# Kernel optimization log

Hardware: AMD Instinct MI355X
Metric: run time of the kernel (lower is better)

Reference implementation:

```python
import jax, jax.numpy as jnp
import numpy as np

N_NODES = 100000
N_EDGES = 1600000
D = 128


def gcn_conv(x, src, dst, ew, W, b, num_nodes):
    """PyG GCNConv: self-loops (weight 1), symmetric deg^{-1/2} normalization,
    linear transform (no bias) then scatter-add aggregation at dst, bias after."""
    loop = jnp.arange(num_nodes)
    s = jnp.concatenate([src, loop])
    d = jnp.concatenate([dst, loop])
    w = jnp.concatenate([ew, jnp.ones((num_nodes,), dtype=x.dtype)])
    deg = jax.ops.segment_sum(w, d, num_segments=num_nodes)
    dinv = jnp.where(deg > 0, jax.lax.rsqrt(deg), 0.0).astype(x.dtype)
    norm = dinv[s] * w * dinv[d]                      # [E+N]
    h = x @ W                                          # [N, out]
    msgs = h[s] * norm[:, None]                        # [E+N, out]
    return jax.ops.segment_sum(msgs, d, num_segments=num_nodes) + b


def setup_inputs() -> dict:
    key = jax.random.key(0)
    ks = jax.random.split(key, 7)
    x = jax.random.normal(ks[0], (N_NODES, D), dtype=jnp.float32)
    edge_index = jax.random.randint(ks[1], (2, N_EDGES), 0, N_NODES, dtype=jnp.int64)
    edge_weight = jax.random.uniform(ks[2], (N_EDGES,), dtype=jnp.float32)
    scale = 1.0 / np.sqrt(D)
    W1 = jax.random.normal(ks[3], (D, D), dtype=jnp.float32) * scale
    b1 = jax.random.normal(ks[4], (D,), dtype=jnp.float32) * 0.01
    W2 = jax.random.normal(ks[5], (D, D), dtype=jnp.float32) * scale
    b2 = jax.random.normal(ks[6], (D,), dtype=jnp.float32) * 0.01
    return {"x": x, "edge_index": edge_index, "edge_weight": edge_weight,
            "W1": W1, "b1": b1, "W2": W2, "b2": b2}


def reference(x, edge_index, edge_weight, W1, b1, W2, b2):
    src, dst = edge_index[0], edge_index[1]
    n = x.shape[0]
    h = gcn_conv(x, src, dst, edge_weight, W1, b1, n)
    h = jax.nn.relu(h)
    h = gcn_conv(h, src, dst, edge_weight, W2, b2, n)
    return jax.nn.relu(h)
```

## Files before the change

kernel.cpp:

```cpp
#include <hip/hip_runtime.h>

#define D 128
#define CAP 64
#define NBSHIFT 7
#define BNODES 128
#define NGRP 8
#define SUBCAP 384

typedef __attribute__((ext_vector_type(8))) short bf16x8;
typedef __attribute__((ext_vector_type(4))) float f32x4;

__device__ __forceinline__ ushort f2bf(float f) {
    uint u = __float_as_uint(f);
    return (ushort)((u + 0x7FFFu + ((u >> 16) & 1u)) >> 16);
}

__global__ __launch_bounds__(256) void k_prep(const float* __restrict__ W1,
                                              const float* __restrict__ W2,
                                              ushort* __restrict__ Wt1,
                                              ushort* __restrict__ Wt2,
                                              int* scnt, int nsc) {
    int i = blockIdx.x * 256 + threadIdx.x;
    if (i < nsc) scnt[i] = 0;
    if (i < 2 * D * D) {
        const float* W = (i < D * D) ? W1 : W2;
        ushort* Wt     = (i < D * D) ? Wt1 : Wt2;
        int j = i & (D * D - 1);
        int k = j >> 7, nn = j & 127;
        Wt[nn * D + k] = f2bf(W[k * D + nn]);
    }
}

__global__ __launch_bounds__(256) void k_bin(const int* __restrict__ src,
                                             const int* __restrict__ dst,
                                             const float* __restrict__ ew,
                                             int* scnt,
                                             uint2* __restrict__ rec, int nE) {
    int e = blockIdx.x * 256 + threadIdx.x;
    if (e >= nE) return;
    int d = dst[e];
    int b = d >> NBSHIFT;
    int g = blockIdx.x & (NGRP - 1);
    int cell = b * NGRP + g;
    int pos = atomicAdd(&scnt[cell], 1);
    if (pos < SUBCAP) {
        uint q = (uint)__float2int_rn(ew[e] * 32767.0f);
        rec[(size_t)cell * SUBCAP + pos] =
            make_uint2(((uint)src[e] << 15) | q, (uint)(d & (BNODES - 1)));
    }
}

__global__ __launch_bounds__(256) void k_build(const uint2* __restrict__ rec,
                                               const int* __restrict__ scnt,
                                               uint* __restrict__ bucket,
                                               int* __restrict__ cnt,
                                               float* __restrict__ dinv, int n) {
    __shared__ uint rows[BNODES * (CAP + 1)];
    __shared__ int  lcnt[BNODES];
    const int tid = threadIdx.x;
    const int b   = blockIdx.x;

    if (tid < BNODES) lcnt[tid] = 0;
    __syncthreads();

#pragma unroll
    for (int g = 0; g < NGRP; ++g) {
        int cell = b * NGRP + g;
        int c = min(scnt[cell], SUBCAP);
        for (int i = tid; i < c; i += 256) {
            uint2 r = rec[(size_t)cell * SUBCAP + i];
            int nl = (int)r.y;
            int p = atomicAdd(&lcnt[nl], 1);
            if (p < CAP) rows[nl * (CAP + 1) + p] = r.x;
        }
    }
    __syncthreads();

    if (tid < BNODES) {
        int node = b * BNODES + tid;
        if (node < n) {
            int c = min(lcnt[tid], CAP);
            float wsum = 0.f;
            for (int i = 0; i < c; ++i)
                wsum += (float)(rows[tid * (CAP + 1) + i] & 32767u);
            dinv[node] = rsqrtf(1.0f + wsum * (1.0f / 32767.0f));
            cnt[node]  = c;
        }
    }
    __syncthreads();

    for (int i = tid; i < BNODES * CAP; i += 256) {
        int nl = i >> 6, sl = i & (CAP - 1);
        int node = b * BNODES + nl;
        if (node < n) bucket[(size_t)node * CAP + sl] = rows[nl * (CAP + 1) + sl];
    }
}

template <bool IN_BF16>
__global__ __launch_bounds__(256) void k_gemm(const void* __restrict__ Xv,
                                              const ushort* __restrict__ Wt,
                                              ushort* __restrict__ H, int n) {
    __shared__ ushort Xs[64][136];
    __shared__ ushort Ws[128][136];
    const int tid  = threadIdx.x;
    const int row0 = blockIdx.x * 64;

#pragma unroll
    for (int p = 0; p < 8; ++p) {
        int f = (p * 256 + tid) * 8;
        int nn = f >> 7, kk = f & 127;
        *(uint4*)(&Ws[nn][kk]) = *(const uint4*)(Wt + f);
    }
    if (IN_BF16) {
        const ushort* X = (const ushort*)Xv;
#pragma unroll
        for (int p = 0; p < 4; ++p) {
            int f = (p * 256 + tid) * 8;
            int r = f >> 7, kk = f & 127;
            uint4 v = {0u, 0u, 0u, 0u};
            if (row0 + r < n) v = *(const uint4*)(X + (size_t)(row0 + r) * D + kk);
            *(uint4*)(&Xs[r][kk]) = v;
        }
    } else {
        const float* X = (const float*)Xv;
#pragma unroll
        for (int p = 0; p < 8; ++p) {
            int f = (p * 256 + tid) * 4;
            int r = f >> 7, kk = f & 127;
            float4 v = {0.f, 0.f, 0.f, 0.f};
            if (row0 + r < n) v = *(const float4*)(X + (size_t)(row0 + r) * D + kk);
            ushort4 o;
            o.x = f2bf(v.x); o.y = f2bf(v.y); o.z = f2bf(v.z); o.w = f2bf(v.w);
            *(ushort4*)(&Xs[r][kk]) = o;
        }
    }
    __syncthreads();

    const int lane = tid & 63;
    const int wave = tid >> 6;
    const int m    = lane & 15;
    const int quad = lane >> 4;
    const int rw   = wave * 16;

    f32x4 acc[8] = {};
#pragma unroll
    for (int kt = 0; kt < 4; ++kt) {
        int k0 = kt * 32 + quad * 8;
        bf16x8 a = *(const bf16x8*)(&Xs[rw + m][k0]);
#pragma unroll
        for (int t = 0; t < 8; ++t) {
            bf16x8 b = *(const bf16x8*)(&Ws[t * 16 + m][k0]);
            acc[t] = __builtin_amdgcn_mfma_f32_16x16x32_bf16(a, b, acc[t], 0, 0, 0);
        }
    }

#pragma unroll
    for (int t = 0; t < 8; ++t) {
#pragma unroll
        for (int r = 0; r < 4; ++r) {
            int row = row0 + rw + quad * 4 + r;
            if (row < n) H[(size_t)row * D + t * 16 + m] = f2bf(acc[t][r]);
        }
    }
}

template <bool OUT_BF16>
__global__ __launch_bounds__(256) void k_agg(const ushort* __restrict__ H,
                                             const int* __restrict__ cnt,
                                             const uint* __restrict__ bucket,
                                             const float* __restrict__ dinv,
                                             const float* __restrict__ bias,
                                             void* __restrict__ outv, int n) {
    int node = blockIdx.x * 4 + (threadIdx.x >> 6);
    if (node >= n) return;
    int lane = threadIdx.x & 63;
    const uint* Hu = (const uint*)H;
    const uint* row = bucket + (size_t)node * CAP;

    float di = dinv[node];
    float c0 = di * (1.0f / 32767.0f);
    uint hs = Hu[(size_t)node * 64 + lane];
    float accx = __uint_as_float(hs << 16) * (di * di);
    float accy = __uint_as_float(hs & 0xFFFF0000u) * (di * di);

    int c = cnt[node];
    int j = 0;
    for (; j + 3 < c; j += 4) {
        uint p0 = row[j],     p1 = row[j + 1];
        uint p2 = row[j + 2], p3 = row[j + 3];
        int s0 = p0 >> 15, s1 = p1 >> 15, s2 = p2 >> 15, s3 = p3 >> 15;
        uint h0 = Hu[(size_t)s0 * 64 + lane];
        uint h1 = Hu[(size_t)s1 * 64 + lane];
        uint h2 = Hu[(size_t)s2 * 64 + lane];
        uint h3 = Hu[(size_t)s3 * 64 + lane];
        float w0 = (float)(p0 & 32767u) * c0 * dinv[s0];
        float w1 = (float)(p1 & 32767u) * c0 * dinv[s1];
        float w2 = (float)(p2 & 32767u) * c0 * dinv[s2];
        float w3 = (float)(p3 & 32767u) * c0 * dinv[s3];
        accx += __uint_as_float(h0 << 16) * w0 + __uint_as_float(h1 << 16) * w1
              + __uint_as_float(h2 << 16) * w2 + __uint_as_float(h3 << 16) * w3;
        accy += __uint_as_float(h0 & 0xFFFF0000u) * w0 + __uint_as_float(h1 & 0xFFFF0000u) * w1
              + __uint_as_float(h2 & 0xFFFF0000u) * w2 + __uint_as_float(h3 & 0xFFFF0000u) * w3;
    }
    for (; j < c; ++j) {
        uint p = row[j];
        int s = p >> 15;
        uint h = Hu[(size_t)s * 64 + lane];
        float w = (float)(p & 32767u) * c0 * dinv[s];
        accx += __uint_as_float(h << 16) * w;
        accy += __uint_as_float(h & 0xFFFF0000u) * w;
    }

    float2 bv = *(const float2*)(bias + lane * 2);
    float rx = fmaxf(accx + bv.x, 0.f);
    float ry = fmaxf(accy + bv.y, 0.f);
    if (OUT_BF16) {
        uint o = (uint)f2bf(rx) | ((uint)f2bf(ry) << 16);
        ((uint*)outv)[(size_t)node * 64 + lane] = o;
    } else {
        float2 r; r.x = rx; r.y = ry;
        ((float2*)outv)[(size_t)node * 64 + lane] = r;
    }
}

extern "C" void kernel_launch(void* const* d_in, const int* in_sizes, int n_in,
                              void* d_out, int out_size, void* d_ws, size_t ws_size,
                              hipStream_t stream) {
    const float* x  = (const float*)d_in[0];
    const int*   ei = (const int*)d_in[1];
    const float* ew = (const float*)d_in[2];
    const float* W1 = (const float*)d_in[3];
    const float* b1 = (const float*)d_in[4];
    const float* W2 = (const float*)d_in[5];
    const float* b2 = (const float*)d_in[6];

    const int n  = in_sizes[0] / D;
    const int nE = in_sizes[2];
    const int* src = ei;
    const int* dst = ei + nE;

    float* out = (float*)d_out;

    const int NB  = (n + BNODES - 1) >> NBSHIFT;
    const int nsc = NB * NGRP;

    uint2*  rec    = (uint2*)d_ws;
    uint*   bucket = (uint*)(rec + (size_t)nsc * SUBCAP);
    ushort* Hbuf   = (ushort*)(bucket + (size_t)n * CAP);
    ushort* Abuf   = Hbuf + (size_t)n * D;
    ushort* Wt1    = Abuf + (size_t)n * D;
    ushort* Wt2    = Wt1 + D * D;
    float*  dinv   = (float*)(Wt2 + D * D);
    int*    cnt    = (int*)(dinv + n);
    int*    scnt   = cnt + n;

    const int nBlkEdge = (nE + 255) / 256;
    const int nBlkWave = (n + 3) / 4;
    const int nBlkGemm = (n + 63) / 64;

    k_prep <<<128,       256, 0, stream>>>(W1, W2, Wt1, Wt2, scnt, nsc);
    k_bin  <<<nBlkEdge,  256, 0, stream>>>(src, dst, ew, scnt, rec, nE);
    k_build<<<NB,        256, 0, stream>>>(rec, scnt, bucket, cnt, dinv, n);

    k_gemm<false><<<nBlkGemm, 256, 0, stream>>>(x, Wt1, Hbuf, n);
    k_agg<true>  <<<nBlkWave, 256, 0, stream>>>(Hbuf, cnt, bucket, dinv, b1, Abuf, n);

    k_gemm<true> <<<nBlkGemm, 256, 0, stream>>>(Abuf, Wt2, Hbuf, n);
    k_agg<false> <<<nBlkWave, 256, 0, stream>>>(Hbuf, cnt, bucket, dinv, b2, out, n);
}
```

Before: 389.0 us.

## Stage edge binning in LDS per block and flush to 256-node cells

Edge binning now runs with a fixed grid of 512 blocks. Each block first buckets its slice of edges into shared memory, one slot per 256-node cell, and then reserves global space once per cell with a single wave-level atomic before writing records out. This cuts the number of global atomics on the cell counters, which previously took one atomic per edge. The build kernel now processes one 256-node cell per block instead of eight sub-cells of 128 nodes. The cell count (391) is hardcoded for 100k nodes, and local overflow falls back to per-edge global atomics, so the code is tied to this input size.

```diff
diff --git a/kernel.cpp b/kernel.cpp
--- a/kernel.cpp
+++ b/kernel.cpp
@@ -2,10 +2,11 @@
 
 #define D 128
 #define CAP 64
-#define NBSHIFT 7
-#define BNODES 128
-#define NGRP 8
-#define SUBCAP 384
+#define NCELL 391
+#define BN2 256
+#define CELLCAP 4608
+#define BCAP 20
+#define ABLK 512
 
 typedef __attribute__((ext_vector_type(8))) short bf16x8;
 typedef __attribute__((ext_vector_type(4))) float f32x4;
@@ -19,9 +20,9 @@
                                               const float* __restrict__ W2,
                                               ushort* __restrict__ Wt1,
                                               ushort* __restrict__ Wt2,
-                                              int* scnt, int nsc) {
+                                              int* scnt) {
     int i = blockIdx.x * 256 + threadIdx.x;
-    if (i < nsc) scnt[i] = 0;
+    if (i < NCELL) scnt[i] = 0;
     if (i < 2 * D * D) {
         const float* W = (i < D * D) ? W1 : W2;
         ushort* Wt     = (i < D * D) ? Wt1 : Wt2;
@@ -35,18 +36,39 @@
                                              const int* __restrict__ dst,
                                              const float* __restrict__ ew,
                                              int* scnt,
-                                             uint2* __restrict__ rec, int nE) {
-    int e = blockIdx.x * 256 + threadIdx.x;
-    if (e >= nE) return;
-    int d = dst[e];
-    int b = d >> NBSHIFT;
-    int g = blockIdx.x & (NGRP - 1);
-    int cell = b * NGRP + g;
-    int pos = atomicAdd(&scnt[cell], 1);
-    if (pos < SUBCAP) {
+                                             uint2* __restrict__ rec, int nE, int epb) {
+    __shared__ uint2 lrec[NCELL * BCAP];
+    __shared__ int   bcnt[NCELL];
+    const int tid = threadIdx.x;
+
+    for (int i = tid; i < NCELL; i += 256) bcnt[i] = 0;
+    __syncthreads();
+
+    int e0 = blockIdx.x * epb;
+    int e1 = min(e0 + epb, nE);
+    for (int e = e0 + tid; e < e1; e += 256) {
+        int d = dst[e];
         uint q = (uint)__float2int_rn(ew[e] * 32767.0f);
-        rec[(size_t)cell * SUBCAP + pos] =
-            make_uint2(((uint)src[e] << 15) | q, (uint)(d & (BNODES - 1)));
+        uint2 r = make_uint2(((uint)src[e] << 15) | q, (uint)(d & (BN2 - 1)));
+        int cell = d >> 8;
+        int p = atomicAdd(&bcnt[cell], 1);
+        if (p < BCAP) {
+            lrec[cell * BCAP + p] = r;
+        } else {
+            int gp = atomicAdd(&scnt[cell], 1);
+            if (gp < CELLCAP) rec[(size_t)cell * CELLCAP + gp] = r;
+        }
+    }
+    __syncthreads();
+
+    const int wave = tid >> 6, lane = tid & 63;
+    for (int cell = wave; cell < NCELL; cell += 4) {
+        int c = min(bcnt[cell], BCAP);
+        int base = 0;
+        if (lane == 0 && c > 0) base = atomicAdd(&scnt[cell], c);
+        base = __shfl(base, 0, 64);
+        if (lane < c)
+            rec[(size_t)cell * CELLCAP + base + lane] = lrec[cell * BCAP + lane];
     }
 }
 
@@ -55,43 +77,39 @@
                                                uint* __restrict__ bucket,
                                                int* __restrict__ cnt,
                                                float* __restrict__ dinv, int n) {
-    __shared__ uint rows[BNODES * (CAP + 1)];
-    __shared__ int  lcnt[BNODES];
+    __shared__ uint rows[BN2 * (CAP + 1)];
+    __shared__ int  lcnt[BN2];
     const int tid = threadIdx.x;
     const int b   = blockIdx.x;
 
-    if (tid < BNODES) lcnt[tid] = 0;
-    __syncthreads();
-
-#pragma unroll
-    for (int g = 0; g < NGRP; ++g) {
-        int cell = b * NGRP + g;
-        int c = min(scnt[cell], SUBCAP);
-        for (int i = tid; i < c; i += 256) {
-            uint2 r = rec[(size_t)cell * SUBCAP + i];
-            int nl = (int)r.y;
-            int p = atomicAdd(&lcnt[nl], 1);
-            if (p < CAP) rows[nl * (CAP + 1) + p] = r.x;
-        }
-    }
-    __syncthreads();
-
-    if (tid < BNODES) {
-        int node = b * BNODES + tid;
+    lcnt[tid] = 0;
+    __syncthreads();
+
+    int c = min(scnt[b], CELLCAP);
+    for (int i = tid; i < c; i += 256) {
+        uint2 r = rec[(size_t)b * CELLCAP + i];
+        int nl = (int)r.y;
+        int p = atomicAdd(&lcnt[nl], 1);
+        if (p < CAP) rows[nl * (CAP + 1) + p] = r.x;
+    }
+    __syncthreads();
+
+    {
+        int node = b * BN2 + tid;
         if (node < n) {
-            int c = min(lcnt[tid], CAP);
+            int cc = min(lcnt[tid], CAP);
             float wsum = 0.f;
-            for (int i = 0; i < c; ++i)
+            for (int i = 0; i < cc; ++i)
                 wsum += (float)(rows[tid * (CAP + 1) + i] & 32767u);
             dinv[node] = rsqrtf(1.0f + wsum * (1.0f / 32767.0f));
-            cnt[node]  = c;
-        }
-    }
-    __syncthreads();
-
-    for (int i = tid; i < BNODES * CAP; i += 256) {
+            cnt[node]  = cc;
+        }
+    }
+    __syncthreads();
+
+    for (int i = tid; i < BN2 * CAP; i += 256) {
         int nl = i >> 6, sl = i & (CAP - 1);
-        int node = b * BNODES + nl;
+        int node = b * BN2 + nl;
         if (node < n) bucket[(size_t)node * CAP + sl] = rows[nl * (CAP + 1) + sl];
     }
 }
@@ -241,11 +259,8 @@
 
     float* out = (float*)d_out;
 
-    const int NB  = (n + BNODES - 1) >> NBSHIFT;
-    const int nsc = NB * NGRP;
-
     uint2*  rec    = (uint2*)d_ws;
-    uint*   bucket = (uint*)(rec + (size_t)nsc * SUBCAP);
+    uint*   bucket = (uint*)(rec + (size_t)NCELL * CELLCAP);
     ushort* Hbuf   = (ushort*)(bucket + (size_t)n * CAP);
     ushort* Abuf   = Hbuf + (size_t)n * D;
     ushort* Wt1    = Abuf + (size_t)n * D;
@@ -254,13 +269,13 @@
     int*    cnt    = (int*)(dinv + n);
     int*    scnt   = cnt + n;
 
-    const int nBlkEdge = (nE + 255) / 256;
+    const int epb      = (nE + ABLK - 1) / ABLK;
     const int nBlkWave = (n + 3) / 4;
     const int nBlkGemm = (n + 63) / 64;
 
-    k_prep <<<128,       256, 0, stream>>>(W1, W2, Wt1, Wt2, scnt, nsc);
-    k_bin  <<<nBlkEdge,  256, 0, stream>>>(src, dst, ew, scnt, rec, nE);
-    k_build<<<NB,        256, 0, stream>>>(rec, scnt, bucket, cnt, dinv, n);
+    k_prep <<<128,   256, 0, stream>>>(W1, W2, Wt1, Wt2, scnt);
+    k_bin  <<<ABLK,  256, 0, stream>>>(src, dst, ew, scnt, rec, nE, epb);
+    k_build<<<NCELL, 256, 0, stream>>>(rec, scnt, bucket, cnt, dinv, n);
 
     k_gemm<false><<<nBlkGemm, 256, 0, stream>>>(x, Wt1, Hbuf, n);
     k_agg<true>  <<<nBlkWave, 256, 0, stream>>>(Hbuf, cnt, bucket, dinv, b1, Abuf, n);
```

New measurement: 950.7 us. +144.4%, slower.
